# Kernel optimization log

Measured on AMD Instinct MI355X. Metric: run time of the kernel, lower is better.

Reference implementation:

```python
import jax, jax.numpy as jnp
import numpy as np
import math

H = 16  # number of heads (init kwarg h)
EPS = 1e-6


def _apply_kernel(x, orf):
    # x: [B, h, L, d_k], orf: [m, d_k]
    m, d_k = orf.shape
    proj = jnp.einsum('bhld,md->bhlm', x, orf) / (d_k ** 0.25)
    norm = jnp.sum(x * x, axis=-1, keepdims=True) / (2.0 * math.sqrt(d_k))
    return (jnp.exp(proj - norm) + EPS) / math.sqrt(m)


def setup_inputs() -> dict:
    key = jax.random.key(0)
    ks = jax.random.split(key, 10)
    B, L, D, m = 4, 4096, 1024, 256
    d_k = D // H
    s = 1.0 / math.sqrt(D)
    return {
        'x': jax.random.normal(ks[0], (B, L, D), jnp.float32),
        'Wq': jax.random.normal(ks[1], (D, D), jnp.float32) * s,
        'bq': jax.random.normal(ks[2], (D,), jnp.float32) * s,
        'Wk': jax.random.normal(ks[3], (D, D), jnp.float32) * s,
        'bk': jax.random.normal(ks[4], (D,), jnp.float32) * s,
        'Wv': jax.random.normal(ks[5], (D, D), jnp.float32) * s,
        'bv': jax.random.normal(ks[6], (D,), jnp.float32) * s,
        'Wo': jax.random.normal(ks[7], (D, D), jnp.float32) * s,
        'bo': jax.random.normal(ks[8], (D,), jnp.float32) * s,
        'orf': jax.random.normal(ks[9], (m, d_k), jnp.float32),
    }


def reference(x, Wq, bq, Wk, bk, Wv, bv, Wo, bo, orf):
    B, L, D = x.shape
    d_k = D // H

    def split(y):  # [B, L, D] -> [B, h, L, d_k]
        return y.reshape(B, L, H, d_k).transpose(0, 2, 1, 3)

    q = split(x @ Wq.T + bq)
    k = split(x @ Wk.T + bk)
    v = split(x @ Wv.T + bv)

    q_phi = _apply_kernel(q, orf)  # [B, h, L, m]
    k_phi = _apply_kernel(k, orf)  # [B, h, L, m]

    # FAVOR+ linear attention: O(L*m*d_k)
    kv = jnp.einsum('bhlm,bhld->bhmd', k_phi, v)      # [B, h, m, d_k]
    ksum = jnp.sum(k_phi, axis=2)                      # [B, h, m]
    num = jnp.einsum('bhlm,bhmd->bhld', q_phi, kv)     # [B, h, L, d_k]
    den = jnp.einsum('bhlm,bhm->bhl', q_phi, ksum)     # [B, h, L]
    out = num / den[..., None]

    out = out.transpose(0, 2, 1, 3).reshape(B, L, D)   # concat heads
    return out @ Wo.T + bo
```

## Files before the change

kernel.cpp:

```cpp
#include <hip/hip_runtime.h>
#include <math.h>

#define HH 16
#define BB 4
#define LL 4096
#define DD 1024
#define DK 64
#define MMF 256
#define EPSF 1e-6f
#define KSCALE (0.35355339059327373f * 1.4426950408889634f)
#define NORMSCALE (0.0625f * 1.4426950408889634f)
#define NSPLIT 8
#define LCH (LL / NSPLIT)

typedef __attribute__((ext_vector_type(8))) short bf16x8;
typedef __attribute__((ext_vector_type(4))) float f32x4;

__device__ __forceinline__ unsigned short f2bf(float f) {
  union { float f; unsigned u; } v; v.f = f;
  unsigned r = v.u + 0x7FFF + ((v.u >> 16) & 1);
  return (unsigned short)(r >> 16);
}
__device__ __forceinline__ float bf2f(unsigned short h) {
  union { unsigned u; float f; } v; v.u = ((unsigned)h) << 16;
  return v.f;
}
__device__ __forceinline__ f32x4 mfma16(bf16x8 a, bf16x8 b, f32x4 c) {
  return __builtin_amdgcn_mfma_f32_16x16x32_bf16(a, b, c, 0, 0, 0);
}
__device__ __forceinline__ void gload16(const unsigned short* g, unsigned short* l) {
  __builtin_amdgcn_global_load_lds(
      (const __attribute__((address_space(1))) void*)g,
      (__attribute__((address_space(3))) void*)l, 16, 0, 0);
}
#define SWZ(row, col) ((col) ^ (((row) & 7) << 3))

__global__ __launch_bounds__(256) void cvt_bf16(
    const float* __restrict__ src, unsigned short* __restrict__ dst, int n) {
  int i = (blockIdx.x * 256 + threadIdx.x) * 4;
  if (i < n) {
    float4 v = *(const float4*)&src[i];
    ushort4 o;
    o.x = f2bf(v.x); o.y = f2bf(v.y); o.z = f2bf(v.z); o.w = f2bf(v.w);
    *(ushort4*)&dst[i] = o;
  }
}

__global__ __launch_bounds__(256) void cvt_orf(
    const float* __restrict__ src, unsigned short* __restrict__ hi,
    unsigned short* __restrict__ lo, int n) {
  int i = blockIdx.x * 256 + threadIdx.x;
  if (i < n) {
    float f = src[i] * KSCALE;
    unsigned short h = f2bf(f);
    hi[i] = h;
    lo[i] = f2bf(f - bf2f(h));
  }
}

template <int MODE>
__global__ __launch_bounds__(256) void gemm_mfma(
    const unsigned short* __restrict__ A, const unsigned short* __restrict__ W,
    const float* __restrict__ bias, float* __restrict__ Cf,
    unsigned short* __restrict__ C1, unsigned short* __restrict__ C2,
    float* __restrict__ Cn, int M, int N, int K) {
  __shared__ __align__(16) unsigned short As[128 * 64];
  __shared__ __align__(16) unsigned short Bs[128 * 64];
  const int tid = threadIdx.x, lane = tid & 63;
  const int w = tid >> 6, wr = w >> 1, wc = w & 1;
  const int g = lane >> 4, li = lane & 15;
  const int flat = blockIdx.y * gridDim.x + blockIdx.x;
  const int xcd = flat & 7, loc = flat >> 3;
  const int m0 = ((xcd << 4) + (loc & 15)) * 128;
  const int n0 = (loc >> 4) * 128;

  f32x4 acc[4][4] = {};
  const int srow8 = lane >> 3;
  const int scol  = ((lane & 7) ^ srow8) << 3;
  const unsigned short* Ag = A + (size_t)(m0 + w * 32 + srow8) * K + scol;
  const unsigned short* Wg = W + (size_t)(n0 + w * 32 + srow8) * K + scol;

  for (int k0 = 0; k0 < K; k0 += 64) {
    __syncthreads();
#pragma unroll
    for (int j = 0; j < 4; ++j) {
      gload16(Ag + (size_t)j * 8 * K + k0, &As[(w * 32 + j * 8) * 64]);
      gload16(Wg + (size_t)j * 8 * K + k0, &Bs[(w * 32 + j * 8) * 64]);
    }
    __syncthreads();
    const int sx = (li & 7) << 3;
#pragma unroll
    for (int kk = 0; kk < 2; ++kk) {
      const int c = (kk * 32 + g * 8) ^ sx;
      bf16x8 af[4], bfr[4];
#pragma unroll
      for (int i = 0; i < 4; ++i)
        af[i] = *(const bf16x8*)&As[(wr * 64 + i * 16 + li) * 64 + c];
#pragma unroll
      for (int j = 0; j < 4; ++j)
        bfr[j] = *(const bf16x8*)&Bs[(wc * 64 + j * 16 + li) * 64 + c];
#pragma unroll
      for (int i = 0; i < 4; ++i)
#pragma unroll
        for (int j = 0; j < 4; ++j)
          acc[i][j] = mfma16(af[i], bfr[j], acc[i][j]);
    }
  }

  if (MODE == 2) {
    const int head = (n0 + wc * 64) >> 6;
#pragma unroll
    for (int i = 0; i < 4; ++i) {
      const int rr = m0 + wr * 64 + i * 16 + 4 * g;
      const int b = rr >> 12, l = rr & 4095;
      const size_t rowb = (size_t)(b * 16 + head) * 4096 + l;
      float np[4] = {0.f, 0.f, 0.f, 0.f};
#pragma unroll
      for (int j = 0; j < 4; ++j) {
        const float bz = bias[n0 + wc * 64 + j * 16 + li];
        const int d = j * 16 + li;
#pragma unroll
        for (int r = 0; r < 4; ++r) {
          float v = acc[i][j][r] + bz;
          np[r] += v * v;
          unsigned short hv = f2bf(v);
          C1[(rowb + r) * 64 + d] = hv;
          C2[(rowb + r) * 64 + d] = f2bf(v - bf2f(hv));
        }
      }
#pragma unroll
      for (int r = 0; r < 4; ++r) {
        float s = np[r];
        s += __shfl_xor(s, 1); s += __shfl_xor(s, 2);
        s += __shfl_xor(s, 4); s += __shfl_xor(s, 8);
        if (li == 0) Cn[rowb + r] = s * NORMSCALE;
      }
    }
  } else {
#pragma unroll
    for (int i = 0; i < 4; ++i) {
      const int rr = m0 + wr * 64 + i * 16 + 4 * g;
#pragma unroll
      for (int j = 0; j < 4; ++j) {
        const int cc = n0 + wc * 64 + j * 16 + li;
        const float bz = bias[cc];
        if (MODE == 1) {
          const int b = rr >> 12, l = rr & 4095;
          ushort4 o;
          o.x = f2bf(acc[i][j][0] + bz); o.y = f2bf(acc[i][j][1] + bz);
          o.z = f2bf(acc[i][j][2] + bz); o.w = f2bf(acc[i][j][3] + bz);
          *(ushort4*)&C1[((size_t)b * 1024 + cc) * 4096 + l] = o;
        } else {
#pragma unroll
          for (int r = 0; r < 4; ++r)
            Cf[(size_t)(rr + r) * N + cc] = acc[i][j][r] + bz;
        }
      }
    }
  }
}

__global__ __launch_bounds__(256, 2) void kv_mfma(
    const unsigned short* __restrict__ khi, const unsigned short* __restrict__ klo,
    const float* __restrict__ knorms, const unsigned short* __restrict__ vt,
    const unsigned short* __restrict__ orfhi, const unsigned short* __restrict__ orflo,
    float* __restrict__ pkv, float* __restrict__ pksum) {
  __shared__ __align__(16) unsigned short KsHi[64 * 64], KsLo[64 * 64];
  __shared__ __align__(16) unsigned short VT[64 * 64], KphiT[64 * 64];
  __shared__ float ns[64];
  const int tid = threadIdx.x, lane = tid & 63, w = tid >> 6;
  const int g = lane >> 4, li = lane & 15;
  const int bh = blockIdx.x, sp = blockIdx.y;
  const int srow8 = lane >> 3;
  const int scol  = ((lane & 7) ^ srow8) << 3;
  const int sx = (li & 7) << 3;

  bf16x8 oh[4][2], ol[4][2];
#pragma unroll
  for (int p = 0; p < 4; ++p)
#pragma unroll
    for (int kk = 0; kk < 2; ++kk) {
      const size_t o = (size_t)(p * 64 + w * 16 + li) * 64 + kk * 32 + g * 8;
      oh[p][kk] = *(const bf16x8*)&orfhi[o];
      ol[p][kk] = *(const bf16x8*)&orflo[o];
    }

  f32x4 kvacc[4][4] = {};
  float ksacc[4][4] = {};

  for (int c = 0; c < LCH / 64; ++c) {
    const int l0 = sp * LCH + c * 64;
    __syncthreads();
    {
      const size_t kb = ((size_t)bh * 4096 + l0 + w * 16 + srow8) * 64 + scol;
      gload16(khi + kb, &KsHi[(w * 16) * 64]);
      gload16(khi + kb + 8 * 64, &KsHi[(w * 16 + 8) * 64]);
      gload16(klo + kb, &KsLo[(w * 16) * 64]);
      gload16(klo + kb + 8 * 64, &KsLo[(w * 16 + 8) * 64]);
      const size_t vb = ((size_t)bh * 64 + w * 16 + srow8) * 4096 + l0 + scol;
      gload16(vt + vb, &VT[(w * 16) * 64]);
      gload16(vt + vb + (size_t)8 * 4096, &VT[(w * 16 + 8) * 64]);
      if (tid < 64) ns[tid] = knorms[(size_t)bh * 4096 + l0 + tid];
    }
    __syncthreads();

#pragma unroll
    for (int p = 0; p < 4; ++p) {
      f32x4 pr[4] = {};
      __builtin_amdgcn_s_setprio(1);
#pragma unroll
      for (int kk = 0; kk < 2; ++kk) {
        const int cx = (kk * 32 + g * 8) ^ sx;
#pragma unroll
        for (int lf = 0; lf < 4; ++lf) {
          const bf16x8 bh2 = *(const bf16x8*)&KsHi[(lf * 16 + li) * 64 + cx];
          const bf16x8 bl2 = *(const bf16x8*)&KsLo[(lf * 16 + li) * 64 + cx];
          pr[lf] = mfma16(oh[p][kk], bh2, pr[lf]);
          pr[lf] = mfma16(oh[p][kk], bl2, pr[lf]);
          pr[lf] = mfma16(ol[p][kk], bh2, pr[lf]);
        }
      }
      __builtin_amdgcn_s_setprio(0);
#pragma unroll
      for (int lf = 0; lf < 4; ++lf) {
        const float nrm = ns[lf * 16 + li];
#pragma unroll
        for (int r = 0; r < 4; ++r) {
          float phi = exp2f(pr[lf][r] - nrm) + EPSF;
          ksacc[p][r] += phi;
          const int row = w * 16 + 4 * g + r;
          KphiT[row * 64 + SWZ(row, lf * 16 + li)] = f2bf(phi);
        }
      }
      __builtin_amdgcn_s_setprio(1);
#pragma unroll
      for (int kk = 0; kk < 2; ++kk) {
        const int cx = (kk * 32 + g * 8) ^ sx;
        const bf16x8 a = *(const bf16x8*)&KphiT[(w * 16 + li) * 64 + cx];
#pragma unroll
        for (int df = 0; df < 4; ++df) {
          const bf16x8 bv = *(const bf16x8*)&VT[(df * 16 + li) * 64 + cx];
          kvacc[p][df] = mfma16(a, bv, kvacc[p][df]);
        }
      }
      __builtin_amdgcn_s_setprio(0);
    }
  }
  float* kvo = pkv + ((size_t)sp * 64 + bh) * (MMF * DK);
#pragma unroll
  for (int p = 0; p < 4; ++p)
#pragma unroll
    for (int df = 0; df < 4; ++df)
#pragma unroll
      for (int r = 0; r < 4; ++r)
        kvo[(p * 64 + w * 16 + 4 * g + r) * DK + df * 16 + li] = kvacc[p][df][r];

  float* kso = pksum + ((size_t)sp * 64 + bh) * MMF;
#pragma unroll
  for (int p = 0; p < 4; ++p)
#pragma unroll
    for (int r = 0; r < 4; ++r) {
      float s = ksacc[p][r];
      s += __shfl_xor(s, 1); s += __shfl_xor(s, 2);
      s += __shfl_xor(s, 4); s += __shfl_xor(s, 8);
      if (li == 0) kso[p * 64 + w * 16 + 4 * g + r] = s;
    }
}

__global__ __launch_bounds__(256) void reduce_parts(
    const float* __restrict__ pkv, unsigned short* __restrict__ kvT,
    const float* __restrict__ pks, float* __restrict__ ksg) {
  const int id = blockIdx.x * 256 + threadIdx.x;
  {
    const int bh = id >> 12, rest = id & 4095;
    const int m0 = (rest >> 6) << 2, d = rest & 63;
    float s0 = 0.f, s1 = 0.f, s2 = 0.f, s3 = 0.f;
#pragma unroll
    for (int sp = 0; sp < NSPLIT; ++sp) {
      const float* p = pkv + (size_t)(sp * 64 + bh) * (MMF * DK) + d;
      s0 += p[(m0 + 0) * DK]; s1 += p[(m0 + 1) * DK];
      s2 += p[(m0 + 2) * DK]; s3 += p[(m0 + 3) * DK];
    }
    ushort4 o;
    o.x = f2bf(s0); o.y = f2bf(s1); o.z = f2bf(s2); o.w = f2bf(s3);
    *(ushort4*)&kvT[((size_t)bh * DK + d) * MMF + m0] = o;
  }
  if (id < 4096) {
    float4 s = {0.f, 0.f, 0.f, 0.f};
#pragma unroll
    for (int sp = 0; sp < NSPLIT; ++sp) {
      float4 v = *(const float4*)&pks[(size_t)sp * 64 * MMF + id * 4];
      s.x += v.x; s.y += v.y; s.z += v.z; s.w += v.w;
    }
    *(float4*)&ksg[id * 4] = s;
  }
}

__global__ __launch_bounds__(512, 4) void qattn_mfma(
    const unsigned short* __restrict__ qhi, const unsigned short* __restrict__ qlo,
    const float* __restrict__ qnorms,
    const unsigned short* __restrict__ orfhi,
    const unsigned short* __restrict__ kvT, const float* __restrict__ ksg,
    unsigned short* __restrict__ attn) {
  __shared__ __align__(16) unsigned short OHi[256 * 64];
  __shared__ __align__(16) unsigned short KvTs[64 * 256];
  __shared__ __align__(16) unsigned short Qphi[8][16 * 64];
  const int tid = threadIdx.x, lane = tid & 63, w = tid >> 6;
  const int g = lane >> 4, li = lane & 15;
  const int bh = blockIdx.x, lb = blockIdx.y;
  const int b = bh >> 4, h = bh & 15;
  const int srow8 = lane >> 3;
  const int scol  = ((lane & 7) ^ srow8) << 3;
  const int sx = (li & 7) << 3;

#pragma unroll
  for (int q = 0; q < 4; ++q) {
    const size_t o = (size_t)(w * 32 + q * 8 + srow8) * 64 + scol;
    gload16(orfhi + o, &OHi[(w * 32 + q * 8) * 64]);
  }
  {
    const int srow2 = lane >> 5;
#pragma unroll
    for (int q = 0; q < 4; ++q) {
      const int d0 = w * 8 + q * 2, dr = d0 + srow2;
      gload16(kvT + ((size_t)bh * DK + dr) * MMF + (((lane & 31) ^ (dr & 7)) << 3),
              &KvTs[d0 * 256]);
    }
  }

  float ksr[4][4];
#pragma unroll
  for (int p = 0; p < 4; ++p)
#pragma unroll
    for (int mf = 0; mf < 4; ++mf)
      ksr[p][mf] = ksg[(size_t)bh * MMF + p * 64 + mf * 16 + li];
  const float4 nr =
      *(const float4*)&qnorms[(size_t)bh * 4096 + lb * 128 + w * 16 + 4 * g];
  bf16x8 qh[2], ql[2];
  {
    const size_t qr = ((size_t)bh * 4096 + lb * 128 + w * 16 + li) * 64 + g * 8;
    qh[0] = *(const bf16x8*)&qhi[qr];
    qh[1] = *(const bf16x8*)&qhi[qr + 32];
    ql[0] = *(const bf16x8*)&qlo[qr];
    ql[1] = *(const bf16x8*)&qlo[qr + 32];
  }
  __syncthreads();

  f32x4 numacc[4] = {};
  float denacc[4] = {};

#pragma unroll
  for (int p = 0; p < 4; ++p) {
    f32x4 pr[4] = {};
    __builtin_amdgcn_s_setprio(1);
#pragma unroll
    for (int kk = 0; kk < 2; ++kk) {
      const int cx = (kk * 32 + g * 8) ^ sx;
#pragma unroll
      for (int mf = 0; mf < 4; ++mf) {
        const int row = p * 64 + mf * 16 + li;
        const bf16x8 bh2 = *(const bf16x8*)&OHi[row * 64 + cx];
        pr[mf] = mfma16(qh[kk], bh2, pr[mf]);
        pr[mf] = mfma16(ql[kk], bh2, pr[mf]);
      }
    }
    __builtin_amdgcn_s_setprio(0);
#pragma unroll
    for (int mf = 0; mf < 4; ++mf) {
      const float ks = ksr[p][mf];
#pragma unroll
      for (int r = 0; r < 4; ++r) {
        float phi = exp2f(pr[mf][r] - nr[r]) + EPSF;
        denacc[r] += phi * ks;
        const int row = 4 * g + r;
        Qphi[w][row * 64 + SWZ(row, mf * 16 + li)] = f2bf(phi);
      }
    }
    __builtin_amdgcn_s_setprio(1);
#pragma unroll
    for (int kk = 0; kk < 2; ++kk) {
      const int cx = (kk * 32 + g * 8) ^ sx;
      const bf16x8 a = *(const bf16x8*)&Qphi[w][li * 64 + cx];
#pragma unroll
      for (int df = 0; df < 4; ++df) {
        const bf16x8 bv = *(const bf16x8*)
            &KvTs[(df * 16 + li) * 256 + (((p * 8 + kk * 4 + g) ^ (li & 7)) << 3)];
        numacc[df] = mfma16(a, bv, numacc[df]);
      }
    }
    __builtin_amdgcn_s_setprio(0);
  }
  float den[4];
#pragma unroll
  for (int r = 0; r < 4; ++r) {
    float s = denacc[r];
    s += __shfl_xor(s, 1); s += __shfl_xor(s, 2);
    s += __shfl_xor(s, 4); s += __shfl_xor(s, 8);
    den[r] = s;
  }
  unsigned short* ab =
      attn + ((size_t)b * 4096 + lb * 128) * 1024 + h * 64;
#pragma unroll
  for (int df = 0; df < 4; ++df)
#pragma unroll
    for (int r = 0; r < 4; ++r)
      ab[(size_t)(w * 16 + 4 * g + r) * 1024 + df * 16 + li] =
          f2bf(numacc[df][r] / den[r]);
}

extern "C" void kernel_launch(void* const* d_in, const int* in_sizes, int n_in,
                              void* d_out, int out_size, void* d_ws, size_t ws_size,
                              hipStream_t stream) {
  (void)in_sizes; (void)n_in; (void)out_size; (void)ws_size;
  const float* x   = (const float*)d_in[0];
  const float* Wq  = (const float*)d_in[1];
  const float* bq  = (const float*)d_in[2];
  const float* Wk  = (const float*)d_in[3];
  const float* bk  = (const float*)d_in[4];
  const float* Wv  = (const float*)d_in[5];
  const float* bv  = (const float*)d_in[6];
  const float* Wo  = (const float*)d_in[7];
  const float* bo  = (const float*)d_in[8];
  const float* orf = (const float*)d_in[9];
  float* out = (float*)d_out;

  const size_t ND = (size_t)BB * LL * DD;
  char* base = (char*)d_ws;
  size_t off = 0;
  auto alloc = [&](size_t bytes) -> char* {
    char* p = base + off;
    off += (bytes + 255) & ~(size_t)255;
    return p;
  };
  unsigned short* wqbf   = (unsigned short*)alloc((size_t)DD * DD * 2);
  unsigned short* wkbf   = (unsigned short*)alloc((size_t)DD * DD * 2);
  unsigned short* wvbf   = (unsigned short*)alloc((size_t)DD * DD * 2);
  unsigned short* wobf   = (unsigned short*)alloc((size_t)DD * DD * 2);
  unsigned short* orfhi  = (unsigned short*)alloc((size_t)MMF * DK * 2);
  unsigned short* orflo  = (unsigned short*)alloc((size_t)MMF * DK * 2);
  unsigned short* xbf    = (unsigned short*)alloc(ND * 2);
  unsigned short* qhi    = (unsigned short*)alloc(ND * 2);
  unsigned short* qlo    = (unsigned short*)alloc(ND * 2);
  unsigned short* khi    = (unsigned short*)alloc(ND * 2);
  unsigned short* klo    = (unsigned short*)alloc(ND * 2);
  unsigned short* vtbuf  = (unsigned short*)alloc(ND * 2);
  float*          qnorms = (float*)alloc((size_t)64 * LL * 4);
  float*          knorms = (float*)alloc((size_t)64 * LL * 4);
  float*          pksum  = (float*)alloc((size_t)NSPLIT * 64 * MMF * 4);
  unsigned short* kvT    = (unsigned short*)alloc((size_t)64 * DK * MMF * 2);
  float*          ksg    = (float*)alloc((size_t)64 * MMF * 4);
  float*          pkv    = (float*)xbf;
  unsigned short* attnbf = khi;

  cvt_bf16<<<16384, 256, 0, stream>>>(x, xbf, (int)ND);
  cvt_bf16<<<1024, 256, 0, stream>>>(Wq, wqbf, DD * DD);
  cvt_bf16<<<1024, 256, 0, stream>>>(Wk, wkbf, DD * DD);
  cvt_bf16<<<1024, 256, 0, stream>>>(Wv, wvbf, DD * DD);
  cvt_bf16<<<1024, 256, 0, stream>>>(Wo, wobf, DD * DD);
  cvt_orf<<<64, 256, 0, stream>>>(orf, orfhi, orflo, MMF * DK);

  dim3 gg(128, 8);
  gemm_mfma<2><<<gg, 256, 0, stream>>>(xbf, wqbf, bq, (float*)0, qhi, qlo,
                                       qnorms, BB * LL, DD, DD);
  gemm_mfma<2><<<gg, 256, 0, stream>>>(xbf, wkbf, bk, (float*)0, khi, klo,
                                       knorms, BB * LL, DD, DD);
  gemm_mfma<1><<<gg, 256, 0, stream>>>(xbf, wvbf, bv, (float*)0, vtbuf,
                                       (unsigned short*)0, (float*)0,
                                       BB * LL, DD, DD);

  kv_mfma<<<dim3(64, NSPLIT), 256, 0, stream>>>(khi, klo, knorms, vtbuf,
                                                orfhi, orflo, pkv, pksum);
  reduce_parts<<<1024, 256, 0, stream>>>(pkv, kvT, pksum, ksg);
  qattn_mfma<<<dim3(64, 32), 512, 0, stream>>>(qhi, qlo, qnorms, orfhi,
                                               kvT, ksg, attnbf);

  gemm_mfma<0><<<gg, 256, 0, stream>>>(attnbf, wobf, bo, out, (unsigned short*)0,
                                       (unsigned short*)0, (float*)0,
                                       BB * LL, DD, DD);
}
```

Before: 347.3 us.

## Stage GEMM epilogues through LDS for vectorized coalesced stores; merge weight conversions

All three GEMM epilogue modes now write accumulators to a padded per-wave LDS tile. The tile is then read back so each lane emits wide, contiguous global stores, replacing scattered 2-byte and 4-byte stores. The aim is fewer, better coalesced write transactions for the Q/K hi-lo outputs, the transposed V output and the final fp32 output. The four weight fp32-to-bf16 conversions are also merged into one launch. The cost is extra LDS traffic and a block barrier after the main loop.

```diff
diff --git a/kernel.cpp b/kernel.cpp
--- a/kernel.cpp
+++ b/kernel.cpp
@@ -15,6 +15,7 @@
 
 typedef __attribute__((ext_vector_type(8))) short bf16x8;
 typedef __attribute__((ext_vector_type(4))) float f32x4;
+typedef __attribute__((ext_vector_type(8))) unsigned short u16x8;
 
 __device__ __forceinline__ unsigned short f2bf(float f) {
   union { float f; unsigned u; } v; v.f = f;
@@ -44,6 +45,26 @@
     o.x = f2bf(v.x); o.y = f2bf(v.y); o.z = f2bf(v.z); o.w = f2bf(v.w);
     *(ushort4*)&dst[i] = o;
   }
+}
+
+__global__ __launch_bounds__(256) void cvt_bf16_w(
+    const float* __restrict__ W0, const float* __restrict__ W1,
+    const float* __restrict__ W2, const float* __restrict__ W3,
+    unsigned short* __restrict__ D0, unsigned short* __restrict__ D1,
+    unsigned short* __restrict__ D2, unsigned short* __restrict__ D3) {
+  const float* s;
+  unsigned short* d;
+  switch (blockIdx.y) {
+    case 0: s = W0; d = D0; break;
+    case 1: s = W1; d = D1; break;
+    case 2: s = W2; d = D2; break;
+    default: s = W3; d = D3; break;
+  }
+  int i = (blockIdx.x * 256 + threadIdx.x) * 4;
+  float4 v = *(const float4*)&s[i];
+  ushort4 o;
+  o.x = f2bf(v.x); o.y = f2bf(v.y); o.z = f2bf(v.z); o.w = f2bf(v.w);
+  *(ushort4*)&d[i] = o;
 }
 
 __global__ __launch_bounds__(256) void cvt_orf(
@@ -64,8 +85,9 @@
     const float* __restrict__ bias, float* __restrict__ Cf,
     unsigned short* __restrict__ C1, unsigned short* __restrict__ C2,
     float* __restrict__ Cn, int M, int N, int K) {
-  __shared__ __align__(16) unsigned short As[128 * 64];
-  __shared__ __align__(16) unsigned short Bs[128 * 64];
+  __shared__ __align__(16) char smem[4 * 32 * 68 * 4];
+  unsigned short* As = (unsigned short*)smem;
+  unsigned short* Bs = (unsigned short*)(smem + 16384);
   const int tid = threadIdx.x, lane = tid & 63;
   const int w = tid >> 6, wr = w >> 1, wc = w & 1;
   const int g = lane >> 4, li = lane & 15;
@@ -107,54 +129,102 @@
     }
   }
 
+  __syncthreads();
+  float* ep = (float*)smem + w * (32 * 68);
+  const int head = (n0 + wc * 64) >> 6;
+  const int rbase = m0 + wr * 64;
+  const int b = rbase >> 12;
+
   if (MODE == 2) {
-    const int head = (n0 + wc * 64) >> 6;
-#pragma unroll
-    for (int i = 0; i < 4; ++i) {
-      const int rr = m0 + wr * 64 + i * 16 + 4 * g;
-      const int b = rr >> 12, l = rr & 4095;
-      const size_t rowb = (size_t)(b * 16 + head) * 4096 + l;
-      float np[4] = {0.f, 0.f, 0.f, 0.f};
-#pragma unroll
-      for (int j = 0; j < 4; ++j) {
-        const float bz = bias[n0 + wc * 64 + j * 16 + li];
-        const int d = j * 16 + li;
-#pragma unroll
-        for (int r = 0; r < 4; ++r) {
-          float v = acc[i][j][r] + bz;
-          np[r] += v * v;
-          unsigned short hv = f2bf(v);
-          C1[(rowb + r) * 64 + d] = hv;
-          C2[(rowb + r) * 64 + d] = f2bf(v - bf2f(hv));
-        }
-      }
-#pragma unroll
-      for (int r = 0; r < 4; ++r) {
-        float s = np[r];
-        s += __shfl_xor(s, 1); s += __shfl_xor(s, 2);
-        s += __shfl_xor(s, 4); s += __shfl_xor(s, 8);
-        if (li == 0) Cn[rowb + r] = s * NORMSCALE;
+#pragma unroll
+    for (int jh = 0; jh < 2; ++jh) {
+#pragma unroll
+      for (int i2 = 0; i2 < 2; ++i2) {
+        const int i = jh * 2 + i2;
+#pragma unroll
+        for (int j = 0; j < 4; ++j) {
+          const float bz = bias[n0 + wc * 64 + j * 16 + li];
+#pragma unroll
+          for (int r = 0; r < 4; ++r)
+            ep[(i2 * 16 + 4 * g + r) * 68 + j * 16 + li] = acc[i][j][r] + bz;
+        }
+      }
+      const int rrow = lane >> 3, cc = lane & 7;
+#pragma unroll
+      for (int p = 0; p < 4; ++p) {
+        const int row = p * 8 + rrow;
+        float v[8];
+        *(f32x4*)&v[0] = *(const f32x4*)&ep[row * 68 + cc * 8];
+        *(f32x4*)&v[4] = *(const f32x4*)&ep[row * 68 + cc * 8 + 4];
+        float np = 0.f;
+        u16x8 hv, lv;
+#pragma unroll
+        for (int e = 0; e < 8; ++e) {
+          float vv = v[e];
+          np += vv * vv;
+          unsigned short h = f2bf(vv);
+          hv[e] = h;
+          lv[e] = f2bf(vv - bf2f(h));
+        }
+        const int lg = (rbase + jh * 32 + row) & 4095;
+        const size_t rowb = (size_t)(b * 16 + head) * 4096 + lg;
+        *(u16x8*)&C1[rowb * 64 + cc * 8] = hv;
+        *(u16x8*)&C2[rowb * 64 + cc * 8] = lv;
+        np += __shfl_xor(np, 1);
+        np += __shfl_xor(np, 2);
+        np += __shfl_xor(np, 4);
+        if (cc == 0) Cn[rowb] = np * NORMSCALE;
+      }
+    }
+  } else if (MODE == 1) {
+#pragma unroll
+    for (int jh = 0; jh < 2; ++jh) {
+#pragma unroll
+      for (int i = 0; i < 4; ++i)
+#pragma unroll
+        for (int j2 = 0; j2 < 2; ++j2) {
+          const int j = jh * 2 + j2;
+          const float bz = bias[n0 + wc * 64 + j * 16 + li];
+          f32x4 t;
+          t[0] = acc[i][j][0] + bz; t[1] = acc[i][j][1] + bz;
+          t[2] = acc[i][j][2] + bz; t[3] = acc[i][j][3] + bz;
+          *(f32x4*)&ep[(j2 * 16 + li) * 68 + i * 16 + 4 * g] = t;
+        }
+      const int rd = lane >> 3, cc = lane & 7;
+#pragma unroll
+      for (int p = 0; p < 4; ++p) {
+        const int dl = p * 8 + rd;
+        float v[8];
+        *(f32x4*)&v[0] = *(const f32x4*)&ep[dl * 68 + cc * 8];
+        *(f32x4*)&v[4] = *(const f32x4*)&ep[dl * 68 + cc * 8 + 4];
+        u16x8 hv;
+#pragma unroll
+        for (int e = 0; e < 8; ++e) hv[e] = f2bf(v[e]);
+        const int dh = jh * 32 + dl;
+        const int lg = rbase & 4095;
+        *(u16x8*)&C1[((size_t)(b * 16 + head) * 64 + dh) * 4096 + lg + cc * 8] = hv;
       }
     }
   } else {
 #pragma unroll
-    for (int i = 0; i < 4; ++i) {
-      const int rr = m0 + wr * 64 + i * 16 + 4 * g;
-#pragma unroll
-      for (int j = 0; j < 4; ++j) {
-        const int cc = n0 + wc * 64 + j * 16 + li;
-        const float bz = bias[cc];
-        if (MODE == 1) {
-          const int b = rr >> 12, l = rr & 4095;
-          ushort4 o;
-          o.x = f2bf(acc[i][j][0] + bz); o.y = f2bf(acc[i][j][1] + bz);
-          o.z = f2bf(acc[i][j][2] + bz); o.w = f2bf(acc[i][j][3] + bz);
-          *(ushort4*)&C1[((size_t)b * 1024 + cc) * 4096 + l] = o;
-        } else {
+    for (int jh = 0; jh < 2; ++jh) {
+#pragma unroll
+      for (int i2 = 0; i2 < 2; ++i2) {
+        const int i = jh * 2 + i2;
+#pragma unroll
+        for (int j = 0; j < 4; ++j) {
+          const float bz = bias[n0 + wc * 64 + j * 16 + li];
 #pragma unroll
           for (int r = 0; r < 4; ++r)
-            Cf[(size_t)(rr + r) * N + cc] = acc[i][j][r] + bz;
-        }
+            ep[(i2 * 16 + 4 * g + r) * 68 + j * 16 + li] = acc[i][j][r] + bz;
+        }
+      }
+      const int rrow = lane >> 4, cc = lane & 15;
+#pragma unroll
+      for (int p = 0; p < 8; ++p) {
+        const int row = p * 4 + rrow;
+        f32x4 v = *(const f32x4*)&ep[row * 68 + cc * 4];
+        *(f32x4*)&Cf[(size_t)(rbase + jh * 32 + row) * 1024 + n0 + wc * 64 + cc * 4] = v;
       }
     }
   }
@@ -453,10 +523,8 @@
   unsigned short* attnbf = khi;
 
   cvt_bf16<<<16384, 256, 0, stream>>>(x, xbf, (int)ND);
-  cvt_bf16<<<1024, 256, 0, stream>>>(Wq, wqbf, DD * DD);
-  cvt_bf16<<<1024, 256, 0, stream>>>(Wk, wkbf, DD * DD);
-  cvt_bf16<<<1024, 256, 0, stream>>>(Wv, wvbf, DD * DD);
-  cvt_bf16<<<1024, 256, 0, stream>>>(Wo, wobf, DD * DD);
+  cvt_bf16_w<<<dim3(1024, 4), 256, 0, stream>>>(Wq, Wk, Wv, Wo,
+                                                wqbf, wkbf, wvbf, wobf);
   cvt_orf<<<64, 256, 0, stream>>>(orf, orfhi, orflo, MMF * DK);
 
   dim3 gg(128, 8);
```

New measurement: 341.9 us. Within noise of the previous version (-1.5%).
